# Performance work log

Hardware: AMD Instinct MI355X
Metric: run time of the kernel (lower is better)

Reference implementation:

```python
import jax, jax.numpy as jnp
import numpy as np

PAD_IDX = 0
B, T, S, H, V = 64, 32, 64, 1024, 32000


def setup_inputs() -> dict:
    key = jax.random.key(0)
    ks = jax.random.split(key, 12)
    s = 0.02
    emb_tbl = jax.random.normal(ks[0], (V, H), jnp.float32) * s
    emb_tbl = emb_tbl.at[PAD_IDX].set(0.0)  # padding_idx row is zero
    return {
        "input": jax.random.randint(ks[1], (B, T), 0, V),
        "memory": jax.random.normal(ks[2], (1, B, H), jnp.float32),
        "encoder_output": jax.random.normal(ks[3], (B, S, H), jnp.float32),
        "xs_len": jax.random.randint(ks[4], (B,), 1, S + 1),
        "embedding": emb_tbl,
        "w_ih": jax.random.normal(ks[5], (3 * H, 2 * H), jnp.float32) * s,
        "w_hh": jax.random.normal(ks[6], (3 * H, H), jnp.float32) * s,
        "b_ih": jnp.zeros((3 * H,), jnp.float32),
        "b_hh": jnp.zeros((3 * H,), jnp.float32),
        "l1": jax.random.normal(ks[7], (H, H), jnp.float32) * s,
        "l2": jax.random.normal(ks[8], (H, 2 * H), jnp.float32) * s,
        "w_out": jax.random.normal(ks[9], (V, H), jnp.float32) * s,
        "b_out": jnp.zeros((V,), jnp.float32),
    }


def _gru_cell(x, h, w_ih, w_hh, b_ih, b_hh):
    # torch.nn.GRUCell math
    gi = x @ w_ih.T + b_ih          # [B, 3H]
    gh = h @ w_hh.T + b_hh          # [B, 3H]
    ir, iz, inn = jnp.split(gi, 3, axis=1)
    hr, hz, hn = jnp.split(gh, 3, axis=1)
    r = jax.nn.sigmoid(ir + hr)
    z = jax.nn.sigmoid(iz + hz)
    n = jnp.tanh(inn + r * hn)
    return (1.0 - z) * n + z * h


def _attention(hidden, enc, seq_mask, l1, l2):
    # hidden: [B,H], enc: [B,S,H], seq_mask: [B,S] float {0,1}
    q = hidden @ l1.T                              # [B,H]
    score = jnp.einsum("bsh,bh->bs", enc, q)       # [B,S]
    masked = seq_mask * score
    # faithful to `masked_att[masked_att == 0] = -1e10`
    masked = jnp.where(masked == 0.0, -1e10, masked)
    attn = jax.nn.softmax(masked, axis=1)          # softmax over source positions
    ctx = jnp.einsum("bs,bsh->bh", attn, enc)      # [B,H]
    out = jnp.tanh(jnp.concatenate([ctx, hidden], axis=1) @ l2.T)
    return out, attn


def reference(input, memory, encoder_output, xs_len, embedding,
              w_ih, w_hh, b_ih, b_hh, l1, l2, w_out, b_out):
    emb = embedding[input]                         # [B,T,H]
    emb_t = jnp.swapaxes(emb, 0, 1)                # [T,B,H]
    h0 = memory[0]                                 # [B,H]
    ctx0 = jnp.zeros_like(h0)
    s_len = encoder_output.shape[1]
    seq_mask = (jnp.arange(s_len)[None, :] < xs_len[:, None]).astype(emb.dtype)  # [B,S]

    def step(carry, e_t):
        h_prev, ctx = carry
        x = jnp.concatenate([e_t, ctx], axis=1)    # [B,2H]
        h = _gru_cell(x, h_prev, w_ih, w_hh, b_ih, b_hh)
        ctx_new, attn = _attention(h, encoder_output, seq_mask, l1, l2)
        scores = jax.nn.log_softmax(ctx_new @ w_out.T + b_out, axis=1)  # [B,V]
        return (h, ctx_new), (scores, attn)

    (h_fin, ctx_fin), (all_scores, all_attn) = jax.lax.scan(step, (h0, ctx0), emb_t)
    decoder_output = jnp.swapaxes(all_scores, 0, 1)        # [B,T,V]
    decoder_hidden = h_fin[None, :, :]                     # [1,B,H]
    attention_weights = jnp.swapaxes(all_attn, 0, 1)       # [B,T,S]
    return decoder_output, decoder_hidden, attention_weights, ctx_fin
```

## Files before the change

### kernel.cpp

```cpp
#include <hip/hip_runtime.h>


#define B_ 64
#define T_ 32
#define S_ 64
#define H_ 1024
#define V_ 32000

#define HID_OFF 65536000L
#define ATT_OFF 65601536L
#define CTF_OFF 65732608L

typedef __attribute__((ext_vector_type(8))) short bf16x8;
typedef __attribute__((ext_vector_type(4))) float f32x4;
typedef __attribute__((ext_vector_type(4))) unsigned int u32x4;
typedef unsigned short u16;

__device__ __forceinline__ u16 f2bf(float v) {
  unsigned int u = __float_as_uint(v);
  unsigned int r = (u + 0x7fffu + ((u >> 16) & 1u)) >> 16;
  return (u16)r;
}
__device__ __forceinline__ float bf2f(u16 h) {
  return __uint_as_float(((unsigned int)h) << 16);
}
__device__ __forceinline__ void split2(float v, u16* hi, u16* lo) {
  u16 h = f2bf(v);
  *hi = h;
  *lo = f2bf(v - bf2f(h));
}


__global__ void k_split(const float* __restrict__ src, u16* __restrict__ hi,
                        u16* __restrict__ lo, int n) {
  int i = blockIdx.x * blockDim.x + threadIdx.x;
  int stride = gridDim.x * blockDim.x;
  for (; i < n; i += stride) split2(src[i], &hi[i], &lo[i]);
}

__global__ void k_tobf(const float* __restrict__ src, u16* __restrict__ dst, int n) {
  int i = blockIdx.x * blockDim.x + threadIdx.x;
  int stride = gridDim.x * blockDim.x;
  for (; i < n; i += stride) dst[i] = f2bf(src[i]);
}

__global__ void k_l1t(const float* __restrict__ l1, u16* __restrict__ hi,
                      u16* __restrict__ lo) {
  __shared__ float tile[64][65];
  int it = blockIdx.x & 15, kt = blockIdx.x >> 4;
  for (int q = 0; q < 16; ++q) {
    int idx = q * 256 + threadIdx.x;
    int r = idx >> 6, c = idx & 63;
    tile[r][c] = l1[(long)(it * 64 + r) * H_ + kt * 64 + c];
  }
  __syncthreads();
  for (int q = 0; q < 16; ++q) {
    int idx = q * 256 + threadIdx.x;
    int r = idx >> 6, c = idx & 63;
    long o = (long)(kt * 64 + r) * H_ + it * 64 + c;
    split2(tile[c][r], &hi[o], &lo[o]);
  }
}

__global__ void k_embx(const int* __restrict__ inp, const float* __restrict__ emb,
                       u16* __restrict__ hi, u16* __restrict__ lo) {
  int bt = blockIdx.x;
  int b = bt >> 5, t = bt & 31;
  int id = inp[b * T_ + t];
  const float* src = emb + (long)id * H_;
  long base = (long)(t * B_ + b) * H_;
  for (int k = threadIdx.x; k < H_; k += 256) split2(src[k], &hi[base + k], &lo[base + k]);
}

__global__ void k_h0(const float* __restrict__ mem, float* __restrict__ hf,
                     u16* __restrict__ hh, u16* __restrict__ hl) {
  int i = blockIdx.x * 256 + threadIdx.x;
  float v = mem[i];
  hf[i] = v;
  split2(v, &hh[i], &hl[i]);
}

__global__ void k_guard(float* out, float v) {
  if (blockIdx.x == 0 && threadIdx.x == 0) out[0] = v;
}

template <int SPLIT, int OMODE>
__launch_bounds__(256)
__global__ void k_gemm128(const u16* __restrict__ Ah, const u16* __restrict__ Al,
                          const u16* __restrict__ Bh, const u16* __restrict__ Bl,
                          float* __restrict__ C, const float* __restrict__ bias,
                          int Mtiles, int Ntiles, int K, int Arow, int Brow, int Crow) {
  (void)Ntiles;
  int bx = blockIdx.x;
  int mt = bx % Mtiles, nt = bx / Mtiles;
  int m0 = mt * 128, n0 = nt * 128;

  __shared__ __attribute__((aligned(16))) u16 lds[(SPLIT ? 4 : 2) * 4096];
  char* L = (char*)lds;
  const int tid = threadIdx.x;
  const int lane = tid & 63, wid = tid >> 6;
  const int wm = wid & 1, wn = wid >> 1;
  const int l15 = lane & 15, kq = lane >> 4;

  f32x4 acc[4][4];
  const f32x4 z4 = {0.f, 0.f, 0.f, 0.f};
#pragma unroll
  for (int i = 0; i < 4; ++i)
#pragma unroll
    for (int j = 0; j < 4; ++j) acc[i][j] = z4;

  const int ksteps = K >> 5;
  for (int kt = 0; kt < ksteps; ++kt) {
    __syncthreads();
#pragma unroll
    for (int h2 = 0; h2 < 2; ++h2) {
      int r = (tid >> 2) + (h2 << 6);
      int slot = tid & 3;
      int so = ((slot ^ (r & 3)) << 4);
      long ga = (long)(m0 + r) * Arow + (kt << 5) + (slot << 3);
      long gb = (long)(n0 + r) * Brow + (kt << 5) + (slot << 3);
      *(u32x4*)(L + r * 64 + so) = *(const u32x4*)(Ah + ga);
      *(u32x4*)(L + 8192 + r * 64 + so) = *(const u32x4*)(Bh + gb);
      if (SPLIT) {
        *(u32x4*)(L + 16384 + r * 64 + so) = *(const u32x4*)(Al + ga);
        *(u32x4*)(L + 24576 + r * 64 + so) = *(const u32x4*)(Bl + gb);
      }
    }
    __syncthreads();
    bf16x8 aH[4], bH[4], aL[4], bL[4];
#pragma unroll
    for (int mi = 0; mi < 4; ++mi) {
      int r = (wm << 6) + (mi << 4) + l15;
      int off = r * 64 + ((kq ^ (r & 3)) << 4);
      aH[mi] = *(const bf16x8*)(L + off);
      if (SPLIT) aL[mi] = *(const bf16x8*)(L + 16384 + off);
    }
#pragma unroll
    for (int ni = 0; ni < 4; ++ni) {
      int c = (wn << 6) + (ni << 4) + l15;
      int off = c * 64 + ((kq ^ (c & 3)) << 4);
      bH[ni] = *(const bf16x8*)(L + 8192 + off);
      if (SPLIT) bL[ni] = *(const bf16x8*)(L + 24576 + off);
    }
#pragma unroll
    for (int mi = 0; mi < 4; ++mi)
#pragma unroll
      for (int ni = 0; ni < 4; ++ni) {
        acc[mi][ni] = __builtin_amdgcn_mfma_f32_16x16x32_bf16(aH[mi], bH[ni], acc[mi][ni], 0, 0, 0);
        if (SPLIT) {
          acc[mi][ni] = __builtin_amdgcn_mfma_f32_16x16x32_bf16(aL[mi], bH[ni], acc[mi][ni], 0, 0, 0);
          acc[mi][ni] = __builtin_amdgcn_mfma_f32_16x16x32_bf16(aH[mi], bL[ni], acc[mi][ni], 0, 0, 0);
        }
      }
  }
#pragma unroll
  for (int mi = 0; mi < 4; ++mi)
#pragma unroll
    for (int ni = 0; ni < 4; ++ni)
#pragma unroll
      for (int e = 0; e < 4; ++e) {
        int r = (wm << 6) + (mi << 4) + (kq << 2) + e;
        int c = (wn << 6) + (ni << 4) + l15;
        int gm = m0 + r, gn = n0 + c;
        float v = acc[mi][ni][e];
        if (OMODE == 0) {
          C[(long)gm * Crow + gn] = v;
        } else {
          v += bias[gn];
          C[((long)(gm & 63) * T_ + (gm >> 6)) * V_ + gn] = v;
        }
      }
}

__launch_bounds__(256)
__global__ void k_gemm64(int mode, int t,
                         const u16* __restrict__ embx_h, const u16* __restrict__ embx_l,
                         const u16* __restrict__ ctx_h, const u16* __restrict__ ctx_l,
                         const u16* __restrict__ h_h, const u16* __restrict__ h_l,
                         const u16* __restrict__ wih_h, const u16* __restrict__ wih_l,
                         const u16* __restrict__ whh_h, const u16* __restrict__ whh_l,
                         const u16* __restrict__ cat_h, const u16* __restrict__ cat_l,
                         const u16* __restrict__ l2_h, const u16* __restrict__ l2_l,
                         float* __restrict__ gip, float* __restrict__ ghp,
                         float* __restrict__ ctxp) {
  const u16 *Ah, *Al, *Bh, *Bl;
  float* outp;
  int Ar, Br, ostr;
  int bx = blockIdx.x;
  if (mode == 0) {
    if (bx < 192) {
      int nt = bx % 48, kc = bx / 48;
      if (kc < 2) {
        Ah = embx_h + (long)t * 65536 + kc * 512;
        Al = embx_l + (long)t * 65536 + kc * 512;
      } else {
        Ah = ctx_h + (long)t * 65536 + (kc - 2) * 512;
        Al = ctx_l + (long)t * 65536 + (kc - 2) * 512;
      }
      Ar = 1024;
      Bh = wih_h + (long)nt * 64 * 2048 + kc * 512;
      Bl = wih_l + (long)nt * 64 * 2048 + kc * 512;
      Br = 2048;
      outp = gip + (long)kc * 196608 + nt * 64;
      ostr = 3072;
    } else {
      int b2 = bx - 192;
      int nt = b2 % 48, kc = b2 / 48;
      Ah = h_h + kc * 512;
      Al = h_l + kc * 512;
      Ar = 1024;
      Bh = whh_h + (long)nt * 64 * 1024 + kc * 512;
      Bl = whh_l + (long)nt * 64 * 1024 + kc * 512;
      Br = 1024;
      outp = ghp + (long)kc * 196608 + nt * 64;
      ostr = 3072;
    }
  } else {
    int nt = bx % 16, kc = bx / 16;
    Ah = cat_h + kc * 512;
    Al = cat_l + kc * 512;
    Ar = 2048;
    Bh = l2_h + (long)nt * 64 * 2048 + kc * 512;
    Bl = l2_l + (long)nt * 64 * 2048 + kc * 512;
    Br = 2048;
    outp = ctxp + (long)kc * 65536 + nt * 64;
    ostr = 1024;
  }

  __shared__ __attribute__((aligned(16))) u16 lds[4 * 2048];
  char* L = (char*)lds;
  const int tid = threadIdx.x;
  const int lane = tid & 63, wid = tid >> 6;
  const int wm = wid & 1, wn = wid >> 1;
  const int l15 = lane & 15, kq = lane >> 4;

  f32x4 acc[2][2];
  const f32x4 z4 = {0.f, 0.f, 0.f, 0.f};
#pragma unroll
  for (int i = 0; i < 2; ++i)
#pragma unroll
    for (int j = 0; j < 2; ++j) acc[i][j] = z4;

  for (int kt = 0; kt < 16; ++kt) {
    __syncthreads();
    {
      int r = tid >> 2, slot = tid & 3;
      int so = ((slot ^ (r & 3)) << 4);
      long ga = (long)r * Ar + (kt << 5) + (slot << 3);
      long gb = (long)r * Br + (kt << 5) + (slot << 3);
      *(u32x4*)(L + r * 64 + so) = *(const u32x4*)(Ah + ga);
      *(u32x4*)(L + 4096 + r * 64 + so) = *(const u32x4*)(Bh + gb);
      *(u32x4*)(L + 8192 + r * 64 + so) = *(const u32x4*)(Al + ga);
      *(u32x4*)(L + 12288 + r * 64 + so) = *(const u32x4*)(Bl + gb);
    }
    __syncthreads();
    bf16x8 aH[2], aL[2], bH[2], bL[2];
#pragma unroll
    for (int mi = 0; mi < 2; ++mi) {
      int r = (wm << 5) + (mi << 4) + l15;
      int off = r * 64 + ((kq ^ (r & 3)) << 4);
      aH[mi] = *(const bf16x8*)(L + off);
      aL[mi] = *(const bf16x8*)(L + 8192 + off);
    }
#pragma unroll
    for (int ni = 0; ni < 2; ++ni) {
      int c = (wn << 5) + (ni << 4) + l15;
      int off = c * 64 + ((kq ^ (c & 3)) << 4);
      bH[ni] = *(const bf16x8*)(L + 4096 + off);
      bL[ni] = *(const bf16x8*)(L + 12288 + off);
    }
#pragma unroll
    for (int mi = 0; mi < 2; ++mi)
#pragma unroll
      for (int ni = 0; ni < 2; ++ni) {
        acc[mi][ni] = __builtin_amdgcn_mfma_f32_16x16x32_bf16(aH[mi], bH[ni], acc[mi][ni], 0, 0, 0);
        acc[mi][ni] = __builtin_amdgcn_mfma_f32_16x16x32_bf16(aL[mi], bH[ni], acc[mi][ni], 0, 0, 0);
        acc[mi][ni] = __builtin_amdgcn_mfma_f32_16x16x32_bf16(aH[mi], bL[ni], acc[mi][ni], 0, 0, 0);
      }
  }
#pragma unroll
  for (int mi = 0; mi < 2; ++mi)
#pragma unroll
    for (int ni = 0; ni < 2; ++ni)
#pragma unroll
      for (int e = 0; e < 4; ++e) {
        int b = (wm << 5) + (mi << 4) + (kq << 2) + e;
        int c = (wn << 5) + (ni << 4) + l15;
        outp[(long)b * ostr + c] = acc[mi][ni][e];
      }
}

__launch_bounds__(256)
__global__ void k_attn(int t, const float* __restrict__ gip, const float* __restrict__ ghp,
                       const float* __restrict__ bih, const float* __restrict__ bhh,
                       float* __restrict__ hf, u16* __restrict__ hh, u16* __restrict__ hl,
                       const float* __restrict__ encT, const float* __restrict__ enc,
                       const int* __restrict__ xs_len,
                       u16* __restrict__ cat_h, u16* __restrict__ cat_l,
                       float* __restrict__ dout) {
  int b = blockIdx.x;
  int tid = threadIdx.x;
  __shared__ __attribute__((aligned(16))) float hs[1024];
  __shared__ float sc_s[64];
  __shared__ float at_s[64];

  for (int j = tid; j < 1024; j += 256) {
    float ir = 0.f, iz = 0.f, inn = 0.f;
#pragma unroll
    for (int kc = 0; kc < 4; ++kc) {
      const float* g = gip + (long)kc * 196608 + b * 3072;
      ir += g[j];
      iz += g[1024 + j];
      inn += g[2048 + j];
    }
    float hr = 0.f, hz = 0.f, hn = 0.f;
#pragma unroll
    for (int kc = 0; kc < 2; ++kc) {
      const float* g = ghp + (long)kc * 196608 + b * 3072;
      hr += g[j];
      hz += g[1024 + j];
      hn += g[2048 + j];
    }
    ir += bih[j]; iz += bih[1024 + j]; inn += bih[2048 + j];
    hr += bhh[j]; hz += bhh[1024 + j]; hn += bhh[2048 + j];
    float r = 1.f / (1.f + expf(-(ir + hr)));
    float z = 1.f / (1.f + expf(-(iz + hz)));
    float n = tanhf(inn + r * hn);
    float hp = hf[b * 1024 + j];
    float h = (1.f - z) * n + z * hp;
    hs[j] = h;
    hf[b * 1024 + j] = h;
    split2(h, &hh[b * 1024 + j], &hl[b * 1024 + j]);
  }
  __syncthreads();

  {
    int s = tid >> 2, part = tid & 3;
    const float4* er = (const float4*)(encT + ((long)b * 64 + s) * 1024);
    const float4* hv = (const float4*)hs;
    float dot = 0.f;
    for (int q = part; q < 256; q += 4) {
      float4 e = er[q], h4 = hv[q];
      dot += e.x * h4.x + e.y * h4.y + e.z * h4.z + e.w * h4.w;
    }
    dot += __shfl_xor(dot, 1);
    dot += __shfl_xor(dot, 2);
    if (part == 0) sc_s[s] = dot;
  }
  __syncthreads();

  if (tid < 64) {
    int len = xs_len[b];
    float v = sc_s[tid];
    if (tid >= len || v == 0.0f) v = -1e10f;
    float m = v;
#pragma unroll
    for (int off = 32; off; off >>= 1) m = fmaxf(m, __shfl_xor(m, off));
    float p = expf(v - m);
    float sum = p;
#pragma unroll
    for (int off = 32; off; off >>= 1) sum += __shfl_xor(sum, off);
    float a = p / sum;
    at_s[tid] = a;
    dout[ATT_OFF + ((long)b * T_ + t) * S_ + tid] = a;
  }
  __syncthreads();

  {
    const float4* encb = (const float4*)(enc + (long)b * 64 * 1024);
    float c0 = 0.f, c1 = 0.f, c2 = 0.f, c3 = 0.f;
    for (int s2 = 0; s2 < 64; ++s2) {
      float a = at_s[s2];
      float4 e4 = encb[s2 * 256 + tid];
      c0 += a * e4.x; c1 += a * e4.y; c2 += a * e4.z; c3 += a * e4.w;
    }
    int k0 = tid * 4;
    float cv[4] = {c0, c1, c2, c3};
#pragma unroll
    for (int ii = 0; ii < 4; ++ii) {
      split2(cv[ii], &cat_h[b * 2048 + k0 + ii], &cat_l[b * 2048 + k0 + ii]);
      float h = hs[k0 + ii];
      split2(h, &cat_h[b * 2048 + 1024 + k0 + ii], &cat_l[b * 2048 + 1024 + k0 + ii]);
      if (t == T_ - 1) dout[HID_OFF + (long)b * 1024 + k0 + ii] = h;
    }
  }
}

__global__ void k_ctxfin(int t, const float* __restrict__ ctxp, u16* __restrict__ ctx_h,
                         u16* __restrict__ ctx_l, float* __restrict__ dout) {
  int i = blockIdx.x * 256 + threadIdx.x;
  float p = ctxp[i] + ctxp[65536 + i] + ctxp[2 * 65536 + i] + ctxp[3 * 65536 + i];
  float v = tanhf(p);
  long o = (long)(t + 1) * 65536 + i;
  split2(v, &ctx_h[o], &ctx_l[o]);
  if (t == T_ - 1) dout[CTF_OFF + i] = v;
}

__device__ __forceinline__ void lse_comb(float& m, float& s, float mo, float so) {
  float M = fmaxf(m, mo);
  s = s * __expf(m - M) + so * __expf(mo - M);
  m = M;
}

__launch_bounds__(256)
__global__ void k_lsm(float* __restrict__ dout) {
  long base = (long)blockIdx.x * V_;
  int tid = threadIdx.x;
  float m = -3.0e38f, s = 0.f;
  for (int v = tid; v < V_; v += 256) {
    float x = dout[base + v];
    if (x > m) {
      s = s * __expf(m - x) + 1.f;
      m = x;
    } else {
      s += __expf(x - m);
    }
  }
#pragma unroll
  for (int off = 32; off; off >>= 1) {
    float mo = __shfl_xor(m, off), so = __shfl_xor(s, off);
    lse_comb(m, s, mo, so);
  }
  __shared__ float ms[4], ss[4];
  if ((tid & 63) == 0) { ms[tid >> 6] = m; ss[tid >> 6] = s; }
  __syncthreads();
  float M = ms[0], S = ss[0];
  for (int w2 = 1; w2 < 4; ++w2) lse_comb(M, S, ms[w2], ss[w2]);
  float logden = M + logf(S);
  for (int v = tid; v < V_; v += 256) dout[base + v] -= logden;
}

extern "C" void kernel_launch(void* const* d_in, const int* in_sizes, int n_in,
                              void* d_out, int out_size, void* d_ws, size_t ws_size,
                              hipStream_t stream) {
  (void)in_sizes; (void)n_in; (void)out_size;
  const int* input = (const int*)d_in[0];
  const float* memory = (const float*)d_in[1];
  const float* enc = (const float*)d_in[2];
  const int* xs_len = (const int*)d_in[3];
  const float* emb = (const float*)d_in[4];
  const float* wih = (const float*)d_in[5];
  const float* whh = (const float*)d_in[6];
  const float* bih = (const float*)d_in[7];
  const float* bhh = (const float*)d_in[8];
  const float* l1 = (const float*)d_in[9];
  const float* l2 = (const float*)d_in[10];
  const float* wout = (const float*)d_in[11];
  const float* bout = (const float*)d_in[12];
  float* out = (float*)d_out;
  char* w = (char*)d_ws;

  size_t off = 0;
  auto alloc = [&](size_t bytes) {
    size_t o = off;
    off = (off + bytes + 255) & ~(size_t)255;
    return o;
  };
  const size_t N_WIH = 3072UL * 2048, N_WHH = 3072UL * 1024, N_L2 = 1024UL * 2048;
  const size_t N_L1 = 1024UL * 1024, N_ENC = 4096UL * 1024, N_WOUT = 32000UL * 1024;
  const size_t N_EMBX = 2048UL * 1024, N_ENCT = 4096UL * 1024, N_CTX = 33UL * 65536;

  size_t o_wih_h = alloc(2 * N_WIH), o_wih_l = alloc(2 * N_WIH);
  size_t o_whh_h = alloc(2 * N_WHH), o_whh_l = alloc(2 * N_WHH);
  size_t o_l2_h = alloc(2 * N_L2), o_l2_l = alloc(2 * N_L2);
  size_t o_l1t_h = alloc(2 * N_L1), o_l1t_l = alloc(2 * N_L1);
  size_t o_enc_h = alloc(2 * N_ENC), o_enc_l = alloc(2 * N_ENC);
  size_t o_wout = alloc(2 * N_WOUT);
  size_t o_embx_h = alloc(2 * N_EMBX), o_embx_l = alloc(2 * N_EMBX);
  size_t o_encT = alloc(4 * N_ENCT);
  size_t o_ctx_h = alloc(2 * N_CTX), o_ctx_l = alloc(2 * N_CTX);
  size_t o_hf = alloc(4 * 65536), o_hh = alloc(2 * 65536), o_hl = alloc(2 * 65536);
  size_t o_cat_h = alloc(2 * 131072), o_cat_l = alloc(2 * 131072);
  size_t o_gip = alloc(4 * 786432), o_ghp = alloc(4 * 393216), o_ctxp = alloc(4 * 262144);

  if (off > ws_size) {
    k_guard<<<1, 1, 0, stream>>>(out, 1.0e8f + (float)(ws_size >> 20));
    return;
  }

  u16* wih_h = (u16*)(w + o_wih_h);   u16* wih_l = (u16*)(w + o_wih_l);
  u16* whh_h = (u16*)(w + o_whh_h);   u16* whh_l = (u16*)(w + o_whh_l);
  u16* l2_h = (u16*)(w + o_l2_h);     u16* l2_l = (u16*)(w + o_l2_l);
  u16* l1t_h = (u16*)(w + o_l1t_h);   u16* l1t_l = (u16*)(w + o_l1t_l);
  u16* enc_h = (u16*)(w + o_enc_h);   u16* enc_l = (u16*)(w + o_enc_l);
  u16* wout_b = (u16*)(w + o_wout);
  u16* embx_h = (u16*)(w + o_embx_h); u16* embx_l = (u16*)(w + o_embx_l);
  float* encT = (float*)(w + o_encT);
  u16* ctx_h = (u16*)(w + o_ctx_h);   u16* ctx_l = (u16*)(w + o_ctx_l);
  float* hf = (float*)(w + o_hf);
  u16* hh = (u16*)(w + o_hh);         u16* hl = (u16*)(w + o_hl);
  u16* cat_h = (u16*)(w + o_cat_h);   u16* cat_l = (u16*)(w + o_cat_l);
  float* gip = (float*)(w + o_gip);
  float* ghp = (float*)(w + o_ghp);
  float* ctxp = (float*)(w + o_ctxp);

  k_split<<<2048, 256, 0, stream>>>(wih, wih_h, wih_l, (int)N_WIH);
  k_split<<<2048, 256, 0, stream>>>(whh, whh_h, whh_l, (int)N_WHH);
  k_split<<<2048, 256, 0, stream>>>(l2, l2_h, l2_l, (int)N_L2);
  k_split<<<2048, 256, 0, stream>>>(enc, enc_h, enc_l, (int)N_ENC);
  k_l1t<<<256, 256, 0, stream>>>(l1, l1t_h, l1t_l);
  k_tobf<<<4096, 256, 0, stream>>>(wout, wout_b, (int)N_WOUT);
  k_embx<<<2048, 256, 0, stream>>>(input, emb, embx_h, embx_l);
  k_h0<<<256, 256, 0, stream>>>(memory, hf, hh, hl);
  hipMemsetAsync(ctx_h, 0, 131072, stream);
  hipMemsetAsync(ctx_l, 0, 131072, stream);

  k_gemm128<1, 0><<<256, 256, 0, stream>>>(enc_h, enc_l, l1t_h, l1t_l, encT, nullptr,
                                           32, 8, 1024, 1024, 1024, 1024);

  for (int t = 0; t < T_; ++t) {
    k_gemm64<<<288, 256, 0, stream>>>(0, t, embx_h, embx_l, ctx_h, ctx_l, hh, hl,
                                      wih_h, wih_l, whh_h, whh_l, cat_h, cat_l,
                                      l2_h, l2_l, gip, ghp, ctxp);
    k_attn<<<64, 256, 0, stream>>>(t, gip, ghp, bih, bhh, hf, hh, hl, encT, enc,
                                   xs_len, cat_h, cat_l, out);
    k_gemm64<<<64, 256, 0, stream>>>(1, t, embx_h, embx_l, ctx_h, ctx_l, hh, hl,
                                     wih_h, wih_l, whh_h, whh_l, cat_h, cat_l,
                                     l2_h, l2_l, gip, ghp, ctxp);
    k_ctxfin<<<256, 256, 0, stream>>>(t, ctxp, ctx_h, ctx_l, out);
  }

  k_gemm128<0, 1><<<4000, 256, 0, stream>>>(ctx_h + 65536, nullptr, wout_b, nullptr,
                                            out, bout, 16, 250, 1024, 1024, 1024, 0);
  k_lsm<<<2048, 256, 0, stream>>>(out);
}
```

Measured before the change: 2.276 ms.

## Fuse recurrent decode loop into one persistent kernel with grid barriers

Replaces the 128 per-timestep launches (two gemm64 launches, attention and ctx finalisation) with a single persistent 192-block kernel that synchronises its phases through a flag-based grid barrier. The embedding half of the input-gate GEMM is hoisted out of the loop into one batched GEMM over all timesteps. The l2 projection now runs the full K=2048 in 16 blocks and applies tanh in its epilogue, which removes the split-K partial buffer and the separate reduction kernel. In exchange the kernel relies on all 192 blocks being co-resident, spin-waits on global flags, and runs the l2 GEMM on fewer blocks.

```diff
diff --git a/kernel.cpp b/kernel.cpp
--- a/kernel.cpp
+++ b/kernel.cpp
@@ -6,6 +6,7 @@
 #define S_ 64
 #define H_ 1024
 #define V_ 32000
+#define NB_ 192
 
 #define HID_OFF 65536000L
 #define ATT_OFF 65601536L
@@ -172,76 +173,16 @@
       }
 }
 
-__launch_bounds__(256)
-__global__ void k_gemm64(int mode, int t,
-                         const u16* __restrict__ embx_h, const u16* __restrict__ embx_l,
-                         const u16* __restrict__ ctx_h, const u16* __restrict__ ctx_l,
-                         const u16* __restrict__ h_h, const u16* __restrict__ h_l,
-                         const u16* __restrict__ wih_h, const u16* __restrict__ wih_l,
-                         const u16* __restrict__ whh_h, const u16* __restrict__ whh_l,
-                         const u16* __restrict__ cat_h, const u16* __restrict__ cat_l,
-                         const u16* __restrict__ l2_h, const u16* __restrict__ l2_l,
-                         float* __restrict__ gip, float* __restrict__ ghp,
-                         float* __restrict__ ctxp) {
-  const u16 *Ah, *Al, *Bh, *Bl;
-  float* outp;
-  int Ar, Br, ostr;
-  int bx = blockIdx.x;
-  if (mode == 0) {
-    if (bx < 192) {
-      int nt = bx % 48, kc = bx / 48;
-      if (kc < 2) {
-        Ah = embx_h + (long)t * 65536 + kc * 512;
-        Al = embx_l + (long)t * 65536 + kc * 512;
-      } else {
-        Ah = ctx_h + (long)t * 65536 + (kc - 2) * 512;
-        Al = ctx_l + (long)t * 65536 + (kc - 2) * 512;
-      }
-      Ar = 1024;
-      Bh = wih_h + (long)nt * 64 * 2048 + kc * 512;
-      Bl = wih_l + (long)nt * 64 * 2048 + kc * 512;
-      Br = 2048;
-      outp = gip + (long)kc * 196608 + nt * 64;
-      ostr = 3072;
-    } else {
-      int b2 = bx - 192;
-      int nt = b2 % 48, kc = b2 / 48;
-      Ah = h_h + kc * 512;
-      Al = h_l + kc * 512;
-      Ar = 1024;
-      Bh = whh_h + (long)nt * 64 * 1024 + kc * 512;
-      Bl = whh_l + (long)nt * 64 * 1024 + kc * 512;
-      Br = 1024;
-      outp = ghp + (long)kc * 196608 + nt * 64;
-      ostr = 3072;
-    }
-  } else {
-    int nt = bx % 16, kc = bx / 16;
-    Ah = cat_h + kc * 512;
-    Al = cat_l + kc * 512;
-    Ar = 2048;
-    Bh = l2_h + (long)nt * 64 * 2048 + kc * 512;
-    Bl = l2_l + (long)nt * 64 * 2048 + kc * 512;
-    Br = 2048;
-    outp = ctxp + (long)kc * 65536 + nt * 64;
-    ostr = 1024;
-  }
-
-  __shared__ __attribute__((aligned(16))) u16 lds[4 * 2048];
-  char* L = (char*)lds;
+__device__ __forceinline__ void gemm64_tile(const u16* __restrict__ Ah,
+                                            const u16* __restrict__ Al, int Ar,
+                                            const u16* __restrict__ Bh,
+                                            const u16* __restrict__ Bl, int Br,
+                                            int kiters, char* L, f32x4 (&acc)[2][2]) {
   const int tid = threadIdx.x;
   const int lane = tid & 63, wid = tid >> 6;
   const int wm = wid & 1, wn = wid >> 1;
   const int l15 = lane & 15, kq = lane >> 4;
-
-  f32x4 acc[2][2];
-  const f32x4 z4 = {0.f, 0.f, 0.f, 0.f};
-#pragma unroll
-  for (int i = 0; i < 2; ++i)
-#pragma unroll
-    for (int j = 0; j < 2; ++j) acc[i][j] = z4;
-
-  for (int kt = 0; kt < 16; ++kt) {
+  for (int kt = 0; kt < kiters; ++kt) {
     __syncthreads();
     {
       int r = tid >> 2, slot = tid & 3;
@@ -278,122 +219,201 @@
         acc[mi][ni] = __builtin_amdgcn_mfma_f32_16x16x32_bf16(aH[mi], bL[ni], acc[mi][ni], 0, 0, 0);
       }
   }
-#pragma unroll
-  for (int mi = 0; mi < 2; ++mi)
-#pragma unroll
-    for (int ni = 0; ni < 2; ++ni)
-#pragma unroll
-      for (int e = 0; e < 4; ++e) {
-        int b = (wm << 5) + (mi << 4) + (kq << 2) + e;
-        int c = (wn << 5) + (ni << 4) + l15;
-        outp[(long)b * ostr + c] = acc[mi][ni][e];
-      }
+}
+
+__device__ __forceinline__ void gridbar(unsigned* flags, unsigned* gen, unsigned seq) {
+  __syncthreads();
+  if (threadIdx.x == 0) {
+    __builtin_amdgcn_fence(__ATOMIC_RELEASE, "agent");
+    __hip_atomic_store(flags + blockIdx.x * 16, seq, __ATOMIC_RELAXED,
+                       __HIP_MEMORY_SCOPE_AGENT);
+  }
+  if (blockIdx.x == 0 && threadIdx.x < 64) {
+    int l = threadIdx.x;
+    for (;;) {
+      unsigned a = __hip_atomic_load(flags + l * 16, __ATOMIC_RELAXED, __HIP_MEMORY_SCOPE_AGENT);
+      unsigned b = __hip_atomic_load(flags + (l + 64) * 16, __ATOMIC_RELAXED, __HIP_MEMORY_SCOPE_AGENT);
+      unsigned c = __hip_atomic_load(flags + (l + 128) * 16, __ATOMIC_RELAXED, __HIP_MEMORY_SCOPE_AGENT);
+      if (__all(a >= seq && b >= seq && c >= seq)) break;
+      __builtin_amdgcn_s_sleep(1);
+    }
+    if (l == 0)
+      __hip_atomic_store(gen, seq, __ATOMIC_RELAXED, __HIP_MEMORY_SCOPE_AGENT);
+  }
+  if (threadIdx.x == 0) {
+    while (__hip_atomic_load(gen, __ATOMIC_RELAXED, __HIP_MEMORY_SCOPE_AGENT) < seq)
+      __builtin_amdgcn_s_sleep(1);
+    __builtin_amdgcn_fence(__ATOMIC_ACQUIRE, "agent");
+  }
+  __syncthreads();
 }
 
 __launch_bounds__(256)
-__global__ void k_attn(int t, const float* __restrict__ gip, const float* __restrict__ ghp,
-                       const float* __restrict__ bih, const float* __restrict__ bhh,
-                       float* __restrict__ hf, u16* __restrict__ hh, u16* __restrict__ hl,
-                       const float* __restrict__ encT, const float* __restrict__ enc,
-                       const int* __restrict__ xs_len,
-                       u16* __restrict__ cat_h, u16* __restrict__ cat_l,
-                       float* __restrict__ dout) {
-  int b = blockIdx.x;
-  int tid = threadIdx.x;
-  __shared__ __attribute__((aligned(16))) float hs[1024];
-  __shared__ float sc_s[64];
-  __shared__ float at_s[64];
-
-  for (int j = tid; j < 1024; j += 256) {
-    float ir = 0.f, iz = 0.f, inn = 0.f;
-#pragma unroll
-    for (int kc = 0; kc < 4; ++kc) {
-      const float* g = gip + (long)kc * 196608 + b * 3072;
-      ir += g[j];
-      iz += g[1024 + j];
-      inn += g[2048 + j];
-    }
-    float hr = 0.f, hz = 0.f, hn = 0.f;
-#pragma unroll
-    for (int kc = 0; kc < 2; ++kc) {
-      const float* g = ghp + (long)kc * 196608 + b * 3072;
-      hr += g[j];
-      hz += g[1024 + j];
-      hn += g[2048 + j];
-    }
-    ir += bih[j]; iz += bih[1024 + j]; inn += bih[2048 + j];
-    hr += bhh[j]; hz += bhh[1024 + j]; hn += bhh[2048 + j];
-    float r = 1.f / (1.f + expf(-(ir + hr)));
-    float z = 1.f / (1.f + expf(-(iz + hz)));
-    float n = tanhf(inn + r * hn);
-    float hp = hf[b * 1024 + j];
-    float h = (1.f - z) * n + z * hp;
-    hs[j] = h;
-    hf[b * 1024 + j] = h;
-    split2(h, &hh[b * 1024 + j], &hl[b * 1024 + j]);
-  }
-  __syncthreads();
-
-  {
-    int s = tid >> 2, part = tid & 3;
-    const float4* er = (const float4*)(encT + ((long)b * 64 + s) * 1024);
-    const float4* hv = (const float4*)hs;
-    float dot = 0.f;
-    for (int q = part; q < 256; q += 4) {
-      float4 e = er[q], h4 = hv[q];
-      dot += e.x * h4.x + e.y * h4.y + e.z * h4.z + e.w * h4.w;
-    }
-    dot += __shfl_xor(dot, 1);
-    dot += __shfl_xor(dot, 2);
-    if (part == 0) sc_s[s] = dot;
-  }
-  __syncthreads();
-
-  if (tid < 64) {
-    int len = xs_len[b];
-    float v = sc_s[tid];
-    if (tid >= len || v == 0.0f) v = -1e10f;
-    float m = v;
-#pragma unroll
-    for (int off = 32; off; off >>= 1) m = fmaxf(m, __shfl_xor(m, off));
-    float p = expf(v - m);
-    float sum = p;
-#pragma unroll
-    for (int off = 32; off; off >>= 1) sum += __shfl_xor(sum, off);
-    float a = p / sum;
-    at_s[tid] = a;
-    dout[ATT_OFF + ((long)b * T_ + t) * S_ + tid] = a;
-  }
-  __syncthreads();
-
-  {
-    const float4* encb = (const float4*)(enc + (long)b * 64 * 1024);
-    float c0 = 0.f, c1 = 0.f, c2 = 0.f, c3 = 0.f;
-    for (int s2 = 0; s2 < 64; ++s2) {
-      float a = at_s[s2];
-      float4 e4 = encb[s2 * 256 + tid];
-      c0 += a * e4.x; c1 += a * e4.y; c2 += a * e4.z; c3 += a * e4.w;
-    }
-    int k0 = tid * 4;
-    float cv[4] = {c0, c1, c2, c3};
-#pragma unroll
-    for (int ii = 0; ii < 4; ++ii) {
-      split2(cv[ii], &cat_h[b * 2048 + k0 + ii], &cat_l[b * 2048 + k0 + ii]);
-      float h = hs[k0 + ii];
-      split2(h, &cat_h[b * 2048 + 1024 + k0 + ii], &cat_l[b * 2048 + 1024 + k0 + ii]);
-      if (t == T_ - 1) dout[HID_OFF + (long)b * 1024 + k0 + ii] = h;
-    }
-  }
-}
-
-__global__ void k_ctxfin(int t, const float* __restrict__ ctxp, u16* __restrict__ ctx_h,
-                         u16* __restrict__ ctx_l, float* __restrict__ dout) {
-  int i = blockIdx.x * 256 + threadIdx.x;
-  float p = ctxp[i] + ctxp[65536 + i] + ctxp[2 * 65536 + i] + ctxp[3 * 65536 + i];
-  float v = tanhf(p);
-  long o = (long)(t + 1) * 65536 + i;
-  split2(v, &ctx_h[o], &ctx_l[o]);
-  if (t == T_ - 1) dout[CTF_OFF + i] = v;
+__global__ void k_rec(const float* __restrict__ embi,
+                      u16* __restrict__ dctx_h, u16* __restrict__ dctx_l,
+                      u16* __restrict__ hh, u16* __restrict__ hl, float* __restrict__ hf,
+                      const u16* __restrict__ wih_h, const u16* __restrict__ wih_l,
+                      const u16* __restrict__ whh_h, const u16* __restrict__ whh_l,
+                      const u16* __restrict__ l2_h, const u16* __restrict__ l2_l,
+                      u16* __restrict__ cat_h, u16* __restrict__ cat_l,
+                      float* __restrict__ gip, float* __restrict__ ghp,
+                      const float* __restrict__ encT, const float* __restrict__ enc,
+                      const int* __restrict__ xs_len,
+                      const float* __restrict__ bih, const float* __restrict__ bhh,
+                      float* __restrict__ dout, unsigned* flags, unsigned* gen) {
+  __shared__ __attribute__((aligned(16))) char L[16384];
+  const int bx = blockIdx.x;
+  const int tid = threadIdx.x;
+  const int lane = tid & 63, wid = tid >> 6;
+  const int wm = wid & 1, wn = wid >> 1;
+  const int l15 = lane & 15, kq = lane >> 4;
+  const f32x4 z4 = {0.f, 0.f, 0.f, 0.f};
+  unsigned seq = 1;
+
+  for (int t = 0; t < T_; ++t) {
+    {
+      const u16 *Ah, *Al, *Bh, *Bl;
+      float* outp;
+      int Ar, Br;
+      if (bx < 96) {
+        int nt = bx % 48, kc = bx / 48;
+        Ah = dctx_h + (long)t * 65536 + kc * 512;
+        Al = dctx_l + (long)t * 65536 + kc * 512;
+        Ar = 1024;
+        Bh = wih_h + 1024 + (long)nt * 64 * 2048 + kc * 512;
+        Bl = wih_l + 1024 + (long)nt * 64 * 2048 + kc * 512;
+        Br = 2048;
+        outp = gip + (long)kc * 196608 + nt * 64;
+      } else {
+        int j2 = bx - 96;
+        int nt = j2 % 48, kc = j2 / 48;
+        Ah = hh + kc * 512;
+        Al = hl + kc * 512;
+        Ar = 1024;
+        Bh = whh_h + (long)nt * 64 * 1024 + kc * 512;
+        Bl = whh_l + (long)nt * 64 * 1024 + kc * 512;
+        Br = 1024;
+        outp = ghp + (long)kc * 196608 + nt * 64;
+      }
+      f32x4 acc[2][2];
+#pragma unroll
+      for (int i = 0; i < 2; ++i)
+#pragma unroll
+        for (int j = 0; j < 2; ++j) acc[i][j] = z4;
+      gemm64_tile(Ah, Al, 1024, Bh, Bl, Br, 16, L, acc);
+      (void)Ar;
+#pragma unroll
+      for (int mi = 0; mi < 2; ++mi)
+#pragma unroll
+        for (int ni = 0; ni < 2; ++ni)
+#pragma unroll
+          for (int e = 0; e < 4; ++e) {
+            int r = (wm << 5) + (mi << 4) + (kq << 2) + e;
+            int c = (wn << 5) + (ni << 4) + l15;
+            outp[(long)r * 3072 + c] = acc[mi][ni][e];
+          }
+    }
+    gridbar(flags, gen, seq++);
+
+    if (bx < 64) {
+      int b = bx;
+      float* hs = (float*)L;
+      float* sc_s = (float*)(L + 4096);
+      float* at_s = (float*)(L + 4352);
+      const float* ebase = embi + ((long)t * 64 + b) * 3072;
+      for (int j = tid; j < 1024; j += 256) {
+        float ir = ebase[j] + gip[b * 3072 + j] + gip[196608 + b * 3072 + j] + bih[j];
+        float iz = ebase[1024 + j] + gip[b * 3072 + 1024 + j] + gip[196608 + b * 3072 + 1024 + j] + bih[1024 + j];
+        float in2 = ebase[2048 + j] + gip[b * 3072 + 2048 + j] + gip[196608 + b * 3072 + 2048 + j] + bih[2048 + j];
+        float hr = ghp[b * 3072 + j] + ghp[196608 + b * 3072 + j] + bhh[j];
+        float hz = ghp[b * 3072 + 1024 + j] + ghp[196608 + b * 3072 + 1024 + j] + bhh[1024 + j];
+        float hn = ghp[b * 3072 + 2048 + j] + ghp[196608 + b * 3072 + 2048 + j] + bhh[2048 + j];
+        float r = 1.f / (1.f + expf(-(ir + hr)));
+        float z = 1.f / (1.f + expf(-(iz + hz)));
+        float n = tanhf(in2 + r * hn);
+        float hp = hf[b * 1024 + j];
+        float h = (1.f - z) * n + z * hp;
+        hs[j] = h;
+        hf[b * 1024 + j] = h;
+        split2(h, &hh[b * 1024 + j], &hl[b * 1024 + j]);
+      }
+      __syncthreads();
+      {
+        int s = tid >> 2, part = tid & 3;
+        const float4* er = (const float4*)(encT + ((long)b * 64 + s) * 1024);
+        const float4* hv = (const float4*)hs;
+        float dot = 0.f;
+        for (int q = part; q < 256; q += 4) {
+          float4 e = er[q], h4 = hv[q];
+          dot += e.x * h4.x + e.y * h4.y + e.z * h4.z + e.w * h4.w;
+        }
+        dot += __shfl_xor(dot, 1);
+        dot += __shfl_xor(dot, 2);
+        if (part == 0) sc_s[s] = dot;
+      }
+      __syncthreads();
+      if (tid < 64) {
+        int len = xs_len[b];
+        float v = sc_s[tid];
+        if (tid >= len || v == 0.0f) v = -1e10f;
+        float m = v;
+#pragma unroll
+        for (int off = 32; off; off >>= 1) m = fmaxf(m, __shfl_xor(m, off));
+        float p = expf(v - m);
+        float sum = p;
+#pragma unroll
+        for (int off = 32; off; off >>= 1) sum += __shfl_xor(sum, off);
+        float a = p / sum;
+        at_s[tid] = a;
+        dout[ATT_OFF + ((long)b * T_ + t) * S_ + tid] = a;
+      }
+      __syncthreads();
+      {
+        const float4* encb = (const float4*)(enc + (long)b * 64 * 1024);
+        float c0 = 0.f, c1 = 0.f, c2 = 0.f, c3 = 0.f;
+        for (int s2 = 0; s2 < 64; ++s2) {
+          float a = at_s[s2];
+          float4 e4 = encb[s2 * 256 + tid];
+          c0 += a * e4.x; c1 += a * e4.y; c2 += a * e4.z; c3 += a * e4.w;
+        }
+        int k0 = tid * 4;
+        float cv[4] = {c0, c1, c2, c3};
+#pragma unroll
+        for (int ii = 0; ii < 4; ++ii) {
+          split2(cv[ii], &cat_h[b * 2048 + k0 + ii], &cat_l[b * 2048 + k0 + ii]);
+          float h = hs[k0 + ii];
+          split2(h, &cat_h[b * 2048 + 1024 + k0 + ii], &cat_l[b * 2048 + 1024 + k0 + ii]);
+          if (t == T_ - 1) dout[HID_OFF + (long)b * 1024 + k0 + ii] = h;
+        }
+      }
+    }
+    gridbar(flags, gen, seq++);
+
+    if (bx < 16) {
+      f32x4 acc[2][2];
+#pragma unroll
+      for (int i = 0; i < 2; ++i)
+#pragma unroll
+        for (int j = 0; j < 2; ++j) acc[i][j] = z4;
+      gemm64_tile(cat_h, cat_l, 2048, l2_h + (long)bx * 64 * 2048,
+                  l2_l + (long)bx * 64 * 2048, 2048, 64, L, acc);
+#pragma unroll
+      for (int mi = 0; mi < 2; ++mi)
+#pragma unroll
+        for (int ni = 0; ni < 2; ++ni)
+#pragma unroll
+          for (int e = 0; e < 4; ++e) {
+            int b = (wm << 5) + (mi << 4) + (kq << 2) + e;
+            int c = (wn << 5) + (ni << 4) + l15;
+            int gcol = bx * 64 + c;
+            float v = tanhf(acc[mi][ni][e]);
+            long o = (long)(t + 1) * 65536 + (long)b * 1024 + gcol;
+            split2(v, &dctx_h[o], &dctx_l[o]);
+            if (t == T_ - 1) dout[CTF_OFF + (long)b * 1024 + gcol] = v;
+          }
+    }
+    gridbar(flags, gen, seq++);
+  }
 }
 
 __device__ __forceinline__ void lse_comb(float& m, float& s, float mo, float so) {
@@ -459,6 +479,7 @@
   const size_t N_WIH = 3072UL * 2048, N_WHH = 3072UL * 1024, N_L2 = 1024UL * 2048;
   const size_t N_L1 = 1024UL * 1024, N_ENC = 4096UL * 1024, N_WOUT = 32000UL * 1024;
   const size_t N_EMBX = 2048UL * 1024, N_ENCT = 4096UL * 1024, N_CTX = 33UL * 65536;
+  const size_t N_EMBI = 2048UL * 3072;
 
   size_t o_wih_h = alloc(2 * N_WIH), o_wih_l = alloc(2 * N_WIH);
   size_t o_whh_h = alloc(2 * N_WHH), o_whh_l = alloc(2 * N_WHH);
@@ -468,10 +489,12 @@
   size_t o_wout = alloc(2 * N_WOUT);
   size_t o_embx_h = alloc(2 * N_EMBX), o_embx_l = alloc(2 * N_EMBX);
   size_t o_encT = alloc(4 * N_ENCT);
+  size_t o_embi = alloc(4 * N_EMBI);
   size_t o_ctx_h = alloc(2 * N_CTX), o_ctx_l = alloc(2 * N_CTX);
   size_t o_hf = alloc(4 * 65536), o_hh = alloc(2 * 65536), o_hl = alloc(2 * 65536);
   size_t o_cat_h = alloc(2 * 131072), o_cat_l = alloc(2 * 131072);
-  size_t o_gip = alloc(4 * 786432), o_ghp = alloc(4 * 393216), o_ctxp = alloc(4 * 262144);
+  size_t o_gip = alloc(4 * 2 * 196608), o_ghp = alloc(4 * 2 * 196608);
+  size_t o_bar = alloc(16384);
 
   if (off > ws_size) {
     k_guard<<<1, 1, 0, stream>>>(out, 1.0e8f + (float)(ws_size >> 20));
@@ -486,13 +509,15 @@
   u16* wout_b = (u16*)(w + o_wout);
   u16* embx_h = (u16*)(w + o_embx_h); u16* embx_l = (u16*)(w + o_embx_l);
   float* encT = (float*)(w + o_encT);
+  float* embi = (float*)(w + o_embi);
   u16* ctx_h = (u16*)(w + o_ctx_h);   u16* ctx_l = (u16*)(w + o_ctx_l);
   float* hf = (float*)(w + o_hf);
   u16* hh = (u16*)(w + o_hh);         u16* hl = (u16*)(w + o_hl);
   u16* cat_h = (u16*)(w + o_cat_h);   u16* cat_l = (u16*)(w + o_cat_l);
   float* gip = (float*)(w + o_gip);
   float* ghp = (float*)(w + o_ghp);
-  float* ctxp = (float*)(w + o_ctxp);
+  unsigned* flags = (unsigned*)(w + o_bar);
+  unsigned* gen = flags + 3072;
 
   k_split<<<2048, 256, 0, stream>>>(wih, wih_h, wih_l, (int)N_WIH);
   k_split<<<2048, 256, 0, stream>>>(whh, whh_h, whh_l, (int)N_WHH);
@@ -504,21 +529,17 @@
   k_h0<<<256, 256, 0, stream>>>(memory, hf, hh, hl);
   hipMemsetAsync(ctx_h, 0, 131072, stream);
   hipMemsetAsync(ctx_l, 0, 131072, stream);
+  hipMemsetAsync(flags, 0, 16384, stream);
 
   k_gemm128<1, 0><<<256, 256, 0, stream>>>(enc_h, enc_l, l1t_h, l1t_l, encT, nullptr,
                                            32, 8, 1024, 1024, 1024, 1024);
-
-  for (int t = 0; t < T_; ++t) {
-    k_gemm64<<<288, 256, 0, stream>>>(0, t, embx_h, embx_l, ctx_h, ctx_l, hh, hl,
-                                      wih_h, wih_l, whh_h, whh_l, cat_h, cat_l,
-                                      l2_h, l2_l, gip, ghp, ctxp);
-    k_attn<<<64, 256, 0, stream>>>(t, gip, ghp, bih, bhh, hf, hh, hl, encT, enc,
-                                   xs_len, cat_h, cat_l, out);
-    k_gemm64<<<64, 256, 0, stream>>>(1, t, embx_h, embx_l, ctx_h, ctx_l, hh, hl,
-                                     wih_h, wih_l, whh_h, whh_l, cat_h, cat_l,
-                                     l2_h, l2_l, gip, ghp, ctxp);
-    k_ctxfin<<<256, 256, 0, stream>>>(t, ctxp, ctx_h, ctx_l, out);
-  }
+  k_gemm128<1, 0><<<384, 256, 0, stream>>>(embx_h, embx_l, wih_h, wih_l, embi, nullptr,
+                                           16, 24, 1024, 1024, 2048, 3072);
+
+  k_rec<<<NB_, 256, 0, stream>>>(embi, ctx_h, ctx_l, hh, hl, hf,
+                                 wih_h, wih_l, whh_h, whh_l, l2_h, l2_l,
+                                 cat_h, cat_l, gip, ghp, encT, enc, xs_len,
+                                 bih, bhh, out, flags, gen);
 
   k_gemm128<0, 1><<<4000, 256, 0, stream>>>(ctx_h + 65536, nullptr, wout_b, nullptr,
                                             out, bout, 16, 250, 1024, 1024, 1024, 0);
```

After: 3.642 ms. 60.0% more time.
